# Kernel optimization log

Measured on AMD Instinct MI355X. Metric: run time of the kernel, lower is better.

Reference implementation:

```python
import jax, jax.numpy as jnp
import numpy as np

N_NODES = 50000
IN_FEAT = 64
HIDDEN = 128
OUT = 10
N_EDGES = 800000


def setup_inputs() -> dict:
    key = jax.random.key(0)
    ks = jax.random.split(key, 8)
    s = lambda fan_in: 1.0 / np.sqrt(fan_in)
    x = jax.random.normal(ks[0], (N_NODES, IN_FEAT), dtype=jnp.float32)
    edge_index = jax.random.randint(ks[1], (2, N_EDGES), 0, N_NODES, dtype=jnp.int32)
    # SAGEConv params: lin_l (neighbor path, has bias) and lin_r (root path, no bias)
    W1l = jax.random.uniform(ks[2], (HIDDEN, IN_FEAT), jnp.float32, -s(IN_FEAT), s(IN_FEAT))
    b1 = jnp.zeros((HIDDEN,), jnp.float32)
    W1r = jax.random.uniform(ks[3], (HIDDEN, IN_FEAT), jnp.float32, -s(IN_FEAT), s(IN_FEAT))
    W2l = jax.random.uniform(ks[4], (OUT, HIDDEN), jnp.float32, -s(HIDDEN), s(HIDDEN))
    b2 = jnp.zeros((OUT,), jnp.float32)
    W2r = jax.random.uniform(ks[5], (OUT, HIDDEN), jnp.float32, -s(HIDDEN), s(HIDDEN))
    return {"x": x, "edge_index": edge_index, "W1l": W1l, "b1": b1, "W1r": W1r,
            "W2l": W2l, "b2": b2, "W2r": W2r}


def _sage_conv(x, src, dst, Wl, b, Wr, num_nodes):
    # mean-aggregate neighbor features (src -> dst), then linear + root linear
    msgs = x[src]                                                    # [E, d]
    agg = jax.ops.segment_sum(msgs, dst, num_segments=num_nodes)     # [N, d]
    cnt = jax.ops.segment_sum(jnp.ones((src.shape[0],), x.dtype), dst,
                              num_segments=num_nodes)                 # [N]
    mean = agg / jnp.maximum(cnt, 1.0)[:, None]
    return mean @ Wl.T + b + x @ Wr.T


def reference(x, edge_index, W1l, b1, W1r, W2l, b2, W2r):
    src, dst = edge_index[0], edge_index[1]
    n = x.shape[0]
    h = jax.nn.relu(_sage_conv(x, src, dst, W1l, b1, W1r, n))   # [N, hidden]
    h = _sage_conv(h, src, dst, W2l, b2, W2r, n)                 # [N, 10]
    # sum over nodes (transpose(0,1) then sum dim=1 == sum over axis 0)
    return jnp.sum(h, axis=0).reshape(1, OUT)
```

## Files before the change

### kernel.cpp

```cpp
#include <hip/hip_runtime.h>
#include <hip/hip_fp8.h>


constexpr int N = 50000;
constexpr int F = 64;
constexpr int H = 128;
constexpr int O = 10;
constexpr int E = 800000;

constexpr int NBUK = 391;
constexpr int CAPC = 2560;
constexpr int ADEPTH = 16;
constexpr int GSTR = 4;
constexpr int SPLIT = 4;

constexpr int NTILE = (N + 63) / 64;
constexpr int NB_TRANS = 391;

constexpr int GBIN_LEN  = NBUK * CAPC;
constexpr int GCUR_LEN  = NBUK * GSTR;
constexpr int MEANH_LEN = N * F / 2;
constexpr int XQ_LEN    = N * F / 4;
constexpr size_t WS_NEED_Q =
    (size_t)GBIN_LEN + GCUR_LEN + N + 2 * H + MEANH_LEN + XQ_LEN;

typedef _Float16 half2v __attribute__((ext_vector_type(2)));

__device__ __forceinline__ unsigned short f32_to_bf16_rne(float f) {
  unsigned u = __float_as_uint(f);
  u += 0x7FFFu + ((u >> 16) & 1u);
  return (unsigned short)(u >> 16);
}

__device__ __forceinline__ unsigned pack2h(float a, float b) {
  half2v h;
  h.x = (_Float16)a;
  h.y = (_Float16)b;
  return __builtin_bit_cast(unsigned, h);
}

__device__ __forceinline__ float dot2h(unsigned a, unsigned b, float c) {
#if __has_builtin(__builtin_amdgcn_fdot2)
  return __builtin_amdgcn_fdot2(__builtin_bit_cast(half2v, a),
                                __builtin_bit_cast(half2v, b), c, false);
#else
  const half2v ha = __builtin_bit_cast(half2v, a);
  const half2v hb = __builtin_bit_cast(half2v, b);
  c = fmaf((float)ha.x, (float)hb.x, c);
  return fmaf((float)ha.y, (float)hb.y, c);
#endif
}

__global__ __launch_bounds__(256) void k_cast(
    const float* __restrict__ x, unsigned* __restrict__ xq4) {
  const int tid = blockIdx.x * blockDim.x + threadIdx.x;
  const int stride = gridDim.x * blockDim.x;
  for (int i = tid; i < N * F / 4; i += stride) {
    const float4 v = reinterpret_cast<const float4*>(x)[i];
    const __hip_fp8_e4m3 a(v.x), b(v.y), c(v.z), d(v.w);
    const unsigned o = (unsigned)a.__x | ((unsigned)b.__x << 8) |
                       ((unsigned)c.__x << 16) | ((unsigned)d.__x << 24);
    __builtin_nontemporal_store(o, xq4 + i);
  }
}

__global__ __launch_bounds__(256) void k_coarse(
    const int* __restrict__ ei, int* __restrict__ gcur,
    unsigned* __restrict__ gbin) {
  __shared__ int scnt[NBUK];
  __shared__ unsigned stage[NBUK][ADEPTH];
  const int tid = threadIdx.x;
  const int lane = tid & 63;
  const int wv = tid >> 6;
  for (int i = tid; i < NBUK; i += 256) scnt[i] = 0;
  __syncthreads();

  const int chunk = E / 256;
  const int base = blockIdx.x * chunk;
  const int end = base + chunk;
  for (int e = base + tid; e < end; e += 256) {
    const int s = ei[e];
    const int d = ei[E + e];
    const int b = d >> 7;
    const unsigned p = ((unsigned)s << 7) | (unsigned)(d & 127);
    const int pos = atomicAdd(&scnt[b], 1);
    if (pos < ADEPTH) {
      stage[b][pos] = p;
    } else {
      const int g = atomicAdd(&gcur[b * GSTR], 1);
      if (g < CAPC) gbin[(size_t)b * CAPC + g] = p;
    }
  }
  __syncthreads();

  for (int b0 = wv * 64 + lane; b0 < NBUK; b0 += 256) {
    int cnt = scnt[b0];
    if (cnt > ADEPTH) cnt = ADEPTH;
    if (cnt > 0) {
      const int gbase = atomicAdd(&gcur[b0 * GSTR], cnt);
      for (int k = 0; k < cnt; ++k) {
        const int g = gbase + k;
        if (g < CAPC) gbin[(size_t)b0 * CAPC + g] = stage[b0][k];
      }
    }
  }
}

template <bool USE_Q>
__global__ __launch_bounds__(512) void k_agg2(
    const float* __restrict__ x, const unsigned char* __restrict__ xq,
    const int* __restrict__ gcur, const unsigned* __restrict__ gbin,
    unsigned short* __restrict__ mean1h, float* __restrict__ wsum) {
  __shared__ int fcnt[32];
  __shared__ float winv_s[32];
  __shared__ unsigned short fbin[32][64];
  const int tid = threadIdx.x;
  const int lane = tid & 63;
  const int wv = __builtin_amdgcn_readfirstlane((int)(tid >> 6));
  const int b = blockIdx.x >> 2;
  const int part = blockIdx.x & 3;
  int mb = gcur[b * GSTR];
  if (mb > CAPC) mb = CAPC;

  if (tid < 32) fcnt[tid] = 0;
  __syncthreads();

  const unsigned* __restrict__ gb = gbin + (size_t)b * CAPC;
  unsigned p0 = 0, p1 = 0, p2 = 0, p3 = 0, p4 = 0;
  bool m0 = false, m1 = false, m2 = false, m3 = false, m4 = false;
#define READF(I, P, M)                                                \
  {                                                                   \
    const bool v = tid + (I) * 512 < mb;                              \
    if (v) (P) = gb[tid + (I) * 512];                                 \
    const int row = (int)((P) & 127u);                                \
    (M) = v && ((row >> 5) == part);                                  \
    if (M) {                                                          \
      const int dl = row & 31;                                        \
      const int pos = atomicAdd(&fcnt[dl], 1);                        \
      if (pos < 46) fbin[dl][pos] = (unsigned short)((P) >> 7);       \
    }                                                                 \
  }
  READF(0, p0, m0) READF(1, p1, m1) READF(2, p2, m2)
  READF(3, p3, m3) READF(4, p4, m4)
#undef READF
  __syncthreads();

  if (tid < 32) {
    const int c = fcnt[tid];
    winv_s[tid] = 1.0f / (float)(c > 0 ? c : 1);
  }
  __syncthreads();

  if (m0) atomicAdd(&wsum[p0 >> 7], winv_s[(p0 & 127u) & 31]);
  if (m1) atomicAdd(&wsum[p1 >> 7], winv_s[(p1 & 127u) & 31]);
  if (m2) atomicAdd(&wsum[p2 >> 7], winv_s[(p2 & 127u) & 31]);
  if (m3) atomicAdd(&wsum[p3 >> 7], winv_s[(p3 & 127u) & 31]);
  if (m4) atomicAdd(&wsum[p4 >> 7], winv_s[(p4 & 127u) & 31]);

  #pragma unroll
  for (int r = 0; r < 4; ++r) {
    const int row = wv * 4 + r;
    const int n = b * 128 + part * 32 + row;
    if (n >= N) break;
    int m = __builtin_amdgcn_readfirstlane(fcnt[row]);
    const float winv = winv_s[row];
    if (m > 46) m = 46;
    const uint4* __restrict__ lq = reinterpret_cast<const uint4*>(&fbin[row][0]);
    const uint4 q0 = lq[0], q1 = lq[1], q2 = lq[2];
    const uint4 q3 = lq[3], q4 = lq[4], q5 = lq[5];
    float acc = 0.f;
#define DO2(U, base)                                                      \
    {                                                                     \
      const unsigned u = __builtin_amdgcn_readfirstlane(U);               \
      int sa = (int)(u & 0xFFFFu), sb = (int)(u >> 16);                   \
      sa = sa < N ? sa : 0;  sb = sb < N ? sb : 0;     \
      float va, vb;                                                       \
      if constexpr (USE_Q) {                                              \
        va = (float)*reinterpret_cast<const __hip_fp8_e4m3*>(             \
                 &xq[(size_t)sa * F + lane]);                             \
        vb = (float)*reinterpret_cast<const __hip_fp8_e4m3*>(             \
                 &xq[(size_t)sb * F + lane]);                             \
      } else {                                                            \
        va = x[(size_t)sa * F + lane];                                    \
        vb = x[(size_t)sb * F + lane];                                    \
      }                                                                   \
      acc += ((base) < m) ? va : 0.f;                                     \
      acc += ((base) + 1 < m) ? vb : 0.f;                                 \
    }
    if (m > 0)  { DO2(q0.x, 0)  DO2(q0.y, 2)  DO2(q0.z, 4)  DO2(q0.w, 6)  }
    if (m > 8)  { DO2(q1.x, 8)  DO2(q1.y, 10) DO2(q1.z, 12) DO2(q1.w, 14) }
    if (m > 16) { DO2(q2.x, 16) DO2(q2.y, 18) DO2(q2.z, 20) DO2(q2.w, 22) }
    if (m > 24) { DO2(q3.x, 24) DO2(q3.y, 26) DO2(q3.z, 28) DO2(q3.w, 30) }
    if (m > 32) { DO2(q4.x, 32) DO2(q4.y, 34) DO2(q4.z, 36) DO2(q4.w, 38) }
    if (m > 40) { DO2(q5.x, 40) DO2(q5.y, 42) DO2(q5.z, 44) }
#undef DO2
    mean1h[(size_t)n * F + lane] = f32_to_bf16_rne(acc * winv);
  }
}

__global__ __launch_bounds__(256) void k_trans(
    const float* __restrict__ x, const unsigned short* __restrict__ mean1h,
    const float* __restrict__ wsum,
    const float* __restrict__ W1l, const float* __restrict__ b1,
    const float* __restrict__ W1r,
    float* __restrict__ S_h, float* __restrict__ S_hw) {
  __shared__ unsigned smem[12288];
  unsigned short* feat_h = reinterpret_cast<unsigned short*>(smem);
  unsigned* wBh = smem + 4096;
  const int tid = threadIdx.x;
  const int tm = tid >> 4;
  const int tj = tid & 15;

  #pragma unroll
  for (int u = 0; u < 8; ++u) {
    const int idx = u * 256 + tid;
    const int jj = idx >> 4;
    const int k4 = idx & 15;
    const float4 vl = *reinterpret_cast<const float4*>(&W1l[jj * F + k4 * 4]);
    const float4 vr = *reinterpret_cast<const float4*>(&W1r[jj * F + k4 * 4]);
    wBh[(k4 * 2 + 0) * 128 + jj] = pack2h(vl.x, vl.y);
    wBh[(k4 * 2 + 1) * 128 + jj] = pack2h(vl.z, vl.w);
    wBh[(32 + k4 * 2 + 0) * 128 + jj] = pack2h(vr.x, vr.y);
    wBh[(32 + k4 * 2 + 1) * 128 + jj] = pack2h(vr.z, vr.w);
  }
  const float4 b1v0 = *reinterpret_cast<const float4*>(&b1[tj * 4]);
  const float4 b1v1 = *reinterpret_cast<const float4*>(&b1[64 + tj * 4]);

  float accS[8] = {0.f, 0.f, 0.f, 0.f, 0.f, 0.f, 0.f, 0.f};
  float accW[8] = {0.f, 0.f, 0.f, 0.f, 0.f, 0.f, 0.f, 0.f};

  for (int t = blockIdx.x; t < NTILE; t += NB_TRANS) {
    const int nbase = t * 64;
    __syncthreads();

    #pragma unroll
    for (int u = 0; u < 8; ++u) {
      const int idx = u * 256 + tid;
      const int nn = idx >> 5;
      const int q = idx & 31;
      const int gn = nbase + nn;
      ushort4 o;
      o.x = 0; o.y = 0; o.z = 0; o.w = 0;
      if (gn < N) {
        float f0, f1, f2, f3;
        if (q < 16) {
          const ushort4 t4 = reinterpret_cast<const ushort4*>(mean1h + (size_t)gn * F)[q];
          f0 = __uint_as_float((unsigned)t4.x << 16);
          f1 = __uint_as_float((unsigned)t4.y << 16);
          f2 = __uint_as_float((unsigned)t4.z << 16);
          f3 = __uint_as_float((unsigned)t4.w << 16);
        } else {
          const float4 v = reinterpret_cast<const float4*>(x + (size_t)gn * F)[q - 16];
          f0 = v.x; f1 = v.y; f2 = v.z; f3 = v.w;
        }
        const unsigned p01 = pack2h(f0, f1);
        const unsigned p23 = pack2h(f2, f3);
        o.x = (unsigned short)(p01 & 0xFFFFu);
        o.y = (unsigned short)(p01 >> 16);
        o.z = (unsigned short)(p23 & 0xFFFFu);
        o.w = (unsigned short)(p23 >> 16);
      }
      const int qs = q ^ ((nn >> 2) & 15);
      *reinterpret_cast<ushort4*>(&feat_h[nn * 128 + qs * 4]) = o;
    }
    __syncthreads();

    float acc[4][8] = {{0.f}};
    #pragma unroll 4
    for (int k4 = 0; k4 < 32; ++k4) {
      uint2 a[4];
      #pragma unroll
      for (int r = 0; r < 4; ++r) {
        const int ks = k4 ^ tm;
        a[r] = *reinterpret_cast<const uint2*>(&feat_h[(tm * 4 + r) * 128 + ks * 4]);
      }
      const uint4 B00 = *reinterpret_cast<const uint4*>(&wBh[(k4 * 2 + 0) * 128 + tj * 4]);
      const uint4 B10 = *reinterpret_cast<const uint4*>(&wBh[(k4 * 2 + 1) * 128 + tj * 4]);
      const uint4 B01 = *reinterpret_cast<const uint4*>(&wBh[(k4 * 2 + 0) * 128 + 64 + tj * 4]);
      const uint4 B11 = *reinterpret_cast<const uint4*>(&wBh[(k4 * 2 + 1) * 128 + 64 + tj * 4]);
      #pragma unroll
      for (int r = 0; r < 4; ++r) {
        acc[r][0] = dot2h(a[r].x, B00.x, acc[r][0]);
        acc[r][0] = dot2h(a[r].y, B10.x, acc[r][0]);
        acc[r][1] = dot2h(a[r].x, B00.y, acc[r][1]);
        acc[r][1] = dot2h(a[r].y, B10.y, acc[r][1]);
        acc[r][2] = dot2h(a[r].x, B00.z, acc[r][2]);
        acc[r][2] = dot2h(a[r].y, B10.z, acc[r][2]);
        acc[r][3] = dot2h(a[r].x, B00.w, acc[r][3]);
        acc[r][3] = dot2h(a[r].y, B10.w, acc[r][3]);
        acc[r][4] = dot2h(a[r].x, B01.x, acc[r][4]);
        acc[r][4] = dot2h(a[r].y, B11.x, acc[r][4]);
        acc[r][5] = dot2h(a[r].x, B01.y, acc[r][5]);
        acc[r][5] = dot2h(a[r].y, B11.y, acc[r][5]);
        acc[r][6] = dot2h(a[r].x, B01.z, acc[r][6]);
        acc[r][6] = dot2h(a[r].y, B11.z, acc[r][6]);
        acc[r][7] = dot2h(a[r].x, B01.w, acc[r][7]);
        acc[r][7] = dot2h(a[r].y, B11.w, acc[r][7]);
      }
    }

    #pragma unroll
    for (int r = 0; r < 4; ++r) {
      const int gn = nbase + tm * 4 + r;
      const bool valid = (gn < N);
      const float wsn = valid ? wsum[gn] : 0.f;
      const float bb[8] = {b1v0.x, b1v0.y, b1v0.z, b1v0.w,
                           b1v1.x, b1v1.y, b1v1.z, b1v1.w};
      #pragma unroll
      for (int c = 0; c < 8; ++c) {
        const float h = valid ? fmaxf(acc[r][c] + bb[c], 0.f) : 0.f;
        accS[c] += h;
        accW[c] = fmaf(wsn, h, accW[c]);
      }
    }
  }

  __syncthreads();
  float* redS = reinterpret_cast<float*>(smem);
  float* redW = reinterpret_cast<float*>(smem) + 2048;
  #pragma unroll
  for (int c = 0; c < 8; ++c) {
    const int j = (c < 4) ? (tj * 4 + c) : (64 + tj * 4 + (c - 4));
    redS[tm * 128 + j] = accS[c];
    redW[tm * 128 + j] = accW[c];
  }
  __syncthreads();
  if (tid < 128) {
    float s = 0.f, w = 0.f;
    #pragma unroll
    for (int m = 0; m < 16; ++m) {
      s += redS[m * 128 + tid];
      w += redW[m * 128 + tid];
    }
    atomicAdd(&S_h[tid], s);
    atomicAdd(&S_hw[tid], w);
  }
}

__global__ __launch_bounds__(64) void k_final(
    const float* __restrict__ S_h, const float* __restrict__ S_hw,
    const float* __restrict__ W2l, const float* __restrict__ b2,
    const float* __restrict__ W2r, float* __restrict__ out) {
  const int j = threadIdx.x;
  if (j < O) {
    float acc = (float)N * b2[j];
    #pragma unroll 8
    for (int k = 0; k < H; ++k)
      acc += S_hw[k] * W2l[j * H + k] + S_h[k] * W2r[j * H + k];
    out[j] = acc;
  }
}

extern "C" void kernel_launch(void* const* d_in, const int* in_sizes, int n_in,
                              void* d_out, int out_size, void* d_ws, size_t ws_size,
                              hipStream_t stream) {
  const float* x   = (const float*)d_in[0];
  const int*   ei  = (const int*)d_in[1];
  const float* W1l = (const float*)d_in[2];
  const float* b1  = (const float*)d_in[3];
  const float* W1r = (const float*)d_in[4];
  const float* W2l = (const float*)d_in[5];
  const float* b2  = (const float*)d_in[6];
  const float* W2r = (const float*)d_in[7];
  float* out = (float*)d_out;
  float* ws  = (float*)d_ws;

  const bool use_q = ws_size >= WS_NEED_Q * 4;

  size_t off = 0;
  unsigned* gbin = (unsigned*)ws; off += GBIN_LEN;
  int* gcur = (int*)(ws + off); off += GCUR_LEN;
  float* wsum = ws + off; off += N;
  float* S_h = ws + off; off += H;
  float* S_hw = ws + off; off += H;
  unsigned short* mean1h = (unsigned short*)(ws + off); off += MEANH_LEN;
  unsigned char* xq = nullptr;
  if (use_q) { xq = (unsigned char*)(ws + off); off += XQ_LEN; }

  (void)hipMemsetAsync(gcur, 0, (size_t)(GCUR_LEN + N + 2 * H) * 4, stream);
  if (use_q)
    hipLaunchKernelGGL(k_cast, dim3(512), dim3(256), 0, stream,
                       x, (unsigned*)xq);
  hipLaunchKernelGGL(k_coarse, dim3(256), dim3(256), 0, stream,
                     ei, gcur, gbin);
  if (use_q) {
    hipLaunchKernelGGL(k_agg2<true>, dim3(NBUK * SPLIT), dim3(512), 0, stream,
                       x, xq, gcur, gbin, mean1h, wsum);
  } else {
    hipLaunchKernelGGL(k_agg2<false>, dim3(NBUK * SPLIT), dim3(512), 0, stream,
                       x, xq, gcur, gbin, mean1h, wsum);
  }
  hipLaunchKernelGGL(k_trans, dim3(NB_TRANS), dim3(256), 0, stream,
                     x, mean1h, wsum, W1l, b1, W1r, S_h, S_hw);
  hipLaunchKernelGGL(k_final, dim3(1), dim3(64), 0, stream,
                     S_h, S_hw, W2l, b2, W2r, out);
}
```

Measured before the change: 134.8 us.

## Replace global wsum atomics with source-bucketed edge bins and LDS reduction

The coarse binning kernel now also buckets every edge by source node, building a second bin array. The aggregation kernel writes per-destination inverse degrees to a global array instead of doing scattered global float atomics into wsum. A new k_wsum kernel reduces those weights per source bucket with LDS atomics. This removes contended global atomics but doubles the binning work and LDS use in k_coarse, adds an extra launch, and shrinks the bucket capacity, so overflow edges could be silently dropped.

```diff
diff --git a/kernel.cpp b/kernel.cpp
--- a/kernel.cpp
+++ b/kernel.cpp
@@ -9,7 +9,7 @@
 constexpr int E = 800000;
 
 constexpr int NBUK = 391;
-constexpr int CAPC = 2560;
+constexpr int CAPC = 2528;
 constexpr int ADEPTH = 16;
 constexpr int GSTR = 4;
 constexpr int SPLIT = 4;
@@ -22,7 +22,7 @@
 constexpr int MEANH_LEN = N * F / 2;
 constexpr int XQ_LEN    = N * F / 4;
 constexpr size_t WS_NEED_Q =
-    (size_t)GBIN_LEN + GCUR_LEN + N + 2 * H + MEANH_LEN + XQ_LEN;
+    (size_t)GBIN_LEN * 2 + GCUR_LEN * 2 + 2 * H + N + N + MEANH_LEN + XQ_LEN;
 
 typedef _Float16 half2v __attribute__((ext_vector_type(2)));
 
@@ -66,13 +66,16 @@
 
 __global__ __launch_bounds__(256) void k_coarse(
     const int* __restrict__ ei, int* __restrict__ gcur,
-    unsigned* __restrict__ gbin) {
+    unsigned* __restrict__ gbin, int* __restrict__ gcur2,
+    unsigned* __restrict__ gbin2) {
   __shared__ int scnt[NBUK];
-  __shared__ unsigned stage[NBUK][ADEPTH];
+  __shared__ unsigned stage[NBUK * ADEPTH];
+  __shared__ int scnt2[NBUK];
+  __shared__ unsigned stage2[NBUK * ADEPTH];
   const int tid = threadIdx.x;
   const int lane = tid & 63;
   const int wv = tid >> 6;
-  for (int i = tid; i < NBUK; i += 256) scnt[i] = 0;
+  for (int i = tid; i < NBUK; i += 256) { scnt[i] = 0; scnt2[i] = 0; }
   __syncthreads();
 
   const int chunk = E / 256;
@@ -81,14 +84,27 @@
   for (int e = base + tid; e < end; e += 256) {
     const int s = ei[e];
     const int d = ei[E + e];
-    const int b = d >> 7;
-    const unsigned p = ((unsigned)s << 7) | (unsigned)(d & 127);
-    const int pos = atomicAdd(&scnt[b], 1);
-    if (pos < ADEPTH) {
-      stage[b][pos] = p;
-    } else {
-      const int g = atomicAdd(&gcur[b * GSTR], 1);
-      if (g < CAPC) gbin[(size_t)b * CAPC + g] = p;
+    {
+      const int b = d >> 7;
+      const unsigned p = ((unsigned)s << 7) | (unsigned)(d & 127);
+      const int pos = atomicAdd(&scnt[b], 1);
+      if (pos < ADEPTH) {
+        stage[b * ADEPTH + pos] = p;
+      } else {
+        const int g = atomicAdd(&gcur[b * GSTR], 1);
+        if (g < CAPC) gbin[(size_t)b * CAPC + g] = p;
+      }
+    }
+    {
+      const int b2 = s >> 7;
+      const unsigned p2 = ((unsigned)d << 7) | (unsigned)(s & 127);
+      const int pos2 = atomicAdd(&scnt2[b2], 1);
+      if (pos2 < ADEPTH) {
+        stage2[b2 * ADEPTH + pos2] = p2;
+      } else {
+        const int g2 = atomicAdd(&gcur2[b2 * GSTR], 1);
+        if (g2 < CAPC) gbin2[(size_t)b2 * CAPC + g2] = p2;
+      }
     }
   }
   __syncthreads();
@@ -100,7 +116,16 @@
       const int gbase = atomicAdd(&gcur[b0 * GSTR], cnt);
       for (int k = 0; k < cnt; ++k) {
         const int g = gbase + k;
-        if (g < CAPC) gbin[(size_t)b0 * CAPC + g] = stage[b0][k];
+        if (g < CAPC) gbin[(size_t)b0 * CAPC + g] = stage[b0 * ADEPTH + k];
+      }
+    }
+    int cnt2 = scnt2[b0];
+    if (cnt2 > ADEPTH) cnt2 = ADEPTH;
+    if (cnt2 > 0) {
+      const int gbase2 = atomicAdd(&gcur2[b0 * GSTR], cnt2);
+      for (int k = 0; k < cnt2; ++k) {
+        const int g2 = gbase2 + k;
+        if (g2 < CAPC) gbin2[(size_t)b0 * CAPC + g2] = stage2[b0 * ADEPTH + k];
       }
     }
   }
@@ -110,7 +135,7 @@
 __global__ __launch_bounds__(512) void k_agg2(
     const float* __restrict__ x, const unsigned char* __restrict__ xq,
     const int* __restrict__ gcur, const unsigned* __restrict__ gbin,
-    unsigned short* __restrict__ mean1h, float* __restrict__ wsum) {
+    unsigned short* __restrict__ mean1h, float* __restrict__ winv_g) {
   __shared__ int fcnt[32];
   __shared__ float winv_s[32];
   __shared__ unsigned short fbin[32][64];
@@ -126,36 +151,30 @@
   __syncthreads();
 
   const unsigned* __restrict__ gb = gbin + (size_t)b * CAPC;
-  unsigned p0 = 0, p1 = 0, p2 = 0, p3 = 0, p4 = 0;
-  bool m0 = false, m1 = false, m2 = false, m3 = false, m4 = false;
-#define READF(I, P, M)                                                \
+#define READF(I)                                                      \
   {                                                                   \
+    unsigned P = 0;                                                   \
     const bool v = tid + (I) * 512 < mb;                              \
-    if (v) (P) = gb[tid + (I) * 512];                                 \
-    const int row = (int)((P) & 127u);                                \
-    (M) = v && ((row >> 5) == part);                                  \
-    if (M) {                                                          \
+    if (v) P = gb[tid + (I) * 512];                                   \
+    const int row = (int)(P & 127u);                                  \
+    if (v && ((row >> 5) == part)) {                                  \
       const int dl = row & 31;                                        \
       const int pos = atomicAdd(&fcnt[dl], 1);                        \
-      if (pos < 46) fbin[dl][pos] = (unsigned short)((P) >> 7);       \
+      if (pos < 46) fbin[dl][pos] = (unsigned short)(P >> 7);         \
     }                                                                 \
   }
-  READF(0, p0, m0) READF(1, p1, m1) READF(2, p2, m2)
-  READF(3, p3, m3) READF(4, p4, m4)
+  READF(0) READF(1) READF(2) READF(3) READF(4)
 #undef READF
   __syncthreads();
 
   if (tid < 32) {
     const int c = fcnt[tid];
-    winv_s[tid] = 1.0f / (float)(c > 0 ? c : 1);
-  }
-  __syncthreads();
-
-  if (m0) atomicAdd(&wsum[p0 >> 7], winv_s[(p0 & 127u) & 31]);
-  if (m1) atomicAdd(&wsum[p1 >> 7], winv_s[(p1 & 127u) & 31]);
-  if (m2) atomicAdd(&wsum[p2 >> 7], winv_s[(p2 & 127u) & 31]);
-  if (m3) atomicAdd(&wsum[p3 >> 7], winv_s[(p3 & 127u) & 31]);
-  if (m4) atomicAdd(&wsum[p4 >> 7], winv_s[(p4 & 127u) & 31]);
+    const float wv_ = 1.0f / (float)(c > 0 ? c : 1);
+    winv_s[tid] = wv_;
+    const int n = b * 128 + part * 32 + tid;
+    if (n < N) winv_g[n] = wv_;
+  }
+  __syncthreads();
 
   #pragma unroll
   for (int r = 0; r < 4; ++r) {
@@ -198,6 +217,30 @@
   }
 }
 
+__global__ __launch_bounds__(512) void k_wsum(
+    const int* __restrict__ gcur2, const unsigned* __restrict__ gbin2,
+    const float* __restrict__ winv_g, float* __restrict__ wsum) {
+  __shared__ float lsum[128];
+  const int tid = threadIdx.x;
+  const int b = blockIdx.x;
+  int mb = gcur2[b * GSTR];
+  if (mb > CAPC) mb = CAPC;
+  if (tid < 128) lsum[tid] = 0.f;
+  __syncthreads();
+  const unsigned* __restrict__ gb = gbin2 + (size_t)b * CAPC;
+  #pragma unroll
+  for (int i = 0; i < 5; ++i) {
+    const int idx = tid + i * 512;
+    if (idx < mb) {
+      const unsigned p = gb[idx];
+      atomicAdd(&lsum[p & 127u], winv_g[p >> 7]);
+    }
+  }
+  __syncthreads();
+  const int n = b * 128 + tid;
+  if (tid < 128 && n < N) wsum[n] = lsum[tid];
+}
+
 __global__ __launch_bounds__(256) void k_trans(
     const float* __restrict__ x, const unsigned short* __restrict__ mean1h,
     const float* __restrict__ wsum,
@@ -369,27 +412,32 @@
 
   size_t off = 0;
   unsigned* gbin = (unsigned*)ws; off += GBIN_LEN;
+  unsigned* gbin2 = (unsigned*)(ws + off); off += GBIN_LEN;
   int* gcur = (int*)(ws + off); off += GCUR_LEN;
-  float* wsum = ws + off; off += N;
+  int* gcur2 = (int*)(ws + off); off += GCUR_LEN;
   float* S_h = ws + off; off += H;
   float* S_hw = ws + off; off += H;
+  float* winv_g = ws + off; off += N;
+  float* wsum = ws + off; off += N;
   unsigned short* mean1h = (unsigned short*)(ws + off); off += MEANH_LEN;
   unsigned char* xq = nullptr;
   if (use_q) { xq = (unsigned char*)(ws + off); off += XQ_LEN; }
 
-  (void)hipMemsetAsync(gcur, 0, (size_t)(GCUR_LEN + N + 2 * H) * 4, stream);
+  (void)hipMemsetAsync(gcur, 0, (size_t)(GCUR_LEN * 2 + 2 * H) * 4, stream);
   if (use_q)
     hipLaunchKernelGGL(k_cast, dim3(512), dim3(256), 0, stream,
                        x, (unsigned*)xq);
   hipLaunchKernelGGL(k_coarse, dim3(256), dim3(256), 0, stream,
-                     ei, gcur, gbin);
+                     ei, gcur, gbin, gcur2, gbin2);
   if (use_q) {
     hipLaunchKernelGGL(k_agg2<true>, dim3(NBUK * SPLIT), dim3(512), 0, stream,
-                       x, xq, gcur, gbin, mean1h, wsum);
+                       x, xq, gcur, gbin, mean1h, winv_g);
   } else {
     hipLaunchKernelGGL(k_agg2<false>, dim3(NBUK * SPLIT), dim3(512), 0, stream,
-                       x, xq, gcur, gbin, mean1h, wsum);
-  }
+                       x, xq, gcur, gbin, mean1h, winv_g);
+  }
+  hipLaunchKernelGGL(k_wsum, dim3(NBUK), dim3(512), 0, stream,
+                     gcur2, gbin2, winv_g, wsum);
   hipLaunchKernelGGL(k_trans, dim3(NB_TRANS), dim3(256), 0, stream,
                      x, mean1h, wsum, W1l, b1, W1r, S_h, S_hw);
   hipLaunchKernelGGL(k_final, dim3(1), dim3(64), 0, stream,
```

Result: faster. 117.1 us (-13.1%).
